# Kernel optimization log

Hardware: AMD Instinct MI355X
Metric: run time of the kernel (lower is better)

The kernel has to match this reference:

```python
import jax, jax.numpy as jnp
import numpy as np

N_HEAD, D_HEAD, D_MODEL = 16, 64, 1024
QLEN, MEMLEN, BSZ = 1024, 1024, 2
KLEN = QLEN + MEMLEN  # rlen == klen
LN_EPS = 1e-5
NEG = -1e30


def _rel_shift(x):
    # x: [qlen, rlen, bsz, n_head] -> Transformer-XL relative shift
    q, r, b, n = x.shape
    zp = jnp.zeros((q, 1, b, n), x.dtype)
    xp = jnp.concatenate([zp, x], axis=1).reshape(r + 1, q, b, n)
    return xp[1:].reshape(q, r, b, n)


def _layer_norm(x, gamma, beta):
    mu = jnp.mean(x, axis=-1, keepdims=True)
    var = jnp.mean((x - mu) ** 2, axis=-1, keepdims=True)
    return (x - mu) * jax.lax.rsqrt(var + LN_EPS) * gamma + beta


def setup_inputs() -> dict:
    key = jax.random.key(0)
    ks = jax.random.split(key, 8)
    w = jax.random.normal(ks[0], (QLEN, BSZ, D_MODEL), jnp.float32)
    r = jax.random.normal(ks[1], (KLEN, D_MODEL), jnp.float32)
    r_w_bias = jax.random.normal(ks[2], (N_HEAD, D_HEAD), jnp.float32) * 0.02
    r_r_bias = jax.random.normal(ks[3], (N_HEAD, D_HEAD), jnp.float32) * 0.02
    mems = jax.random.normal(ks[4], (MEMLEN, BSZ, D_MODEL), jnp.float32)
    W_qkv = jax.random.normal(ks[5], (D_MODEL, 3 * N_HEAD * D_HEAD), jnp.float32) * 0.02
    W_r = jax.random.normal(ks[6], (D_MODEL, N_HEAD * D_HEAD), jnp.float32) * 0.02
    W_o = jax.random.normal(ks[7], (N_HEAD * D_HEAD, D_MODEL), jnp.float32) * 0.02
    ln_gamma = jnp.ones((D_MODEL,), jnp.float32)
    ln_beta = jnp.zeros((D_MODEL,), jnp.float32)
    # causal mask with memory: key j visible to query i iff j <= i + MEMLEN (True = keep)
    attn_mask = jnp.arange(KLEN)[None, :] <= (jnp.arange(QLEN)[:, None] + MEMLEN)
    return {"w": w, "r": r, "r_w_bias": r_w_bias, "r_r_bias": r_r_bias,
            "mems": mems, "attn_mask": attn_mask, "W_qkv": W_qkv, "W_r": W_r,
            "W_o": W_o, "ln_gamma": ln_gamma, "ln_beta": ln_beta}


def reference(w, r, r_w_bias, r_r_bias, mems, attn_mask, W_qkv, W_r, W_o, ln_gamma, ln_beta):
    qlen, bsz = w.shape[0], w.shape[1]
    scale = 1.0 / (D_HEAD ** 0.5)
    cat = jnp.concatenate([mems, w], axis=0)            # [klen, b, d_model]
    klen = cat.shape[0]
    w_heads = cat @ W_qkv                                # [klen, b, 3*H*D]
    r_head_k = (r @ W_r).reshape(-1, N_HEAD, D_HEAD)     # [rlen, H, D]
    w_head_q, w_head_k, w_head_v = jnp.split(w_heads, 3, axis=-1)
    w_head_q = w_head_q[-qlen:].reshape(qlen, bsz, N_HEAD, D_HEAD)
    w_head_k = w_head_k.reshape(klen, bsz, N_HEAD, D_HEAD)
    w_head_v = w_head_v.reshape(klen, bsz, N_HEAD, D_HEAD)
    AC = jnp.einsum('ibnd,jbnd->ijbn', w_head_q + r_w_bias, w_head_k)
    BD = jnp.einsum('ibnd,jnd->ijbn', w_head_q + r_r_bias, r_head_k)
    BD = _rel_shift(BD)
    attn_score = (AC + BD) * scale                       # [q, k, b, n]
    attn_score = jnp.where(attn_mask[:, :, None, None], attn_score, NEG)
    attn_prob = jax.nn.softmax(attn_score, axis=1)
    attn_vec = jnp.einsum('ijbn,jbnd->ibnd', attn_prob, w_head_v)
    attn_vec = attn_vec.reshape(qlen, bsz, N_HEAD * D_HEAD)
    attn_out = attn_vec @ W_o                            # [q, b, d_model]
    return _layer_norm(w + attn_out, ln_gamma, ln_beta)
```

## Files before the change

kernel.cpp:

```cpp
#include <hip/hip_runtime.h>
#include <hip/hip_bf16.h>

#define NHEAD 16
#define DHEAD 64
#define DMODEL 1024
#define QLEN 1024
#define MEMLEN 1024
#define BSZ 2
#define KLEN 2048
#define LN_EPS 1e-5f

typedef __hip_bfloat16 bf16;
typedef __attribute__((ext_vector_type(8))) short short8;
typedef __attribute__((ext_vector_type(4))) float f32x4;

__device__ __forceinline__ float b2f(bf16 x) { return __bfloat162float(x); }
__device__ __forceinline__ bf16 f2b(float x) { return __float2bfloat16(x); }
__device__ __forceinline__ short f2bs(float f) {
    bf16 h = __float2bfloat16(f);
    return *reinterpret_cast<short*>(&h);
}
__device__ __forceinline__ float s2f(short s) {
    bf16 h = *reinterpret_cast<bf16*>(&s);
    return __bfloat162float(h);
}

#define MFMA16(a, b, c) __builtin_amdgcn_mfma_f32_16x16x32_bf16(a, b, c, 0, 0, 0)

#define AS1 __attribute__((address_space(1)))
#define AS3 __attribute__((address_space(3)))
__device__ __forceinline__ void gld16(const bf16* g, bf16* l) {
    __builtin_amdgcn_global_load_lds((const AS1 void*)(uintptr_t)g,
                                     (AS3 void*)(uint32_t)(uintptr_t)l, 16, 0, 0);
}

__global__ __launch_bounds__(256)
void conv_all(const float* __restrict__ mems, const float* __restrict__ w,
              const float* __restrict__ r, bf16* __restrict__ Abf,
              bf16* __restrict__ rbf) {
    const int id = blockIdx.x;
    const float* src;
    bf16* dst;
    int off;
    if (id < 2048)      { src = mems; dst = Abf;                      off = id; }
    else if (id < 4096) { src = w;    dst = Abf + (size_t)2048 * 1024; off = id - 2048; }
    else                { src = r;    dst = rbf;                      off = id - 4096; }
    int i = off * 256 + threadIdx.x;
    const float4 v = reinterpret_cast<const float4*>(src)[i];
    bf16 o[4] = {f2b(v.x), f2b(v.y), f2b(v.z), f2b(v.w)};
    reinterpret_cast<ulong1*>(dst)[i] = *reinterpret_cast<ulong1*>(o);
}

__global__ __launch_bounds__(256)
void conv_wT_all(const float* __restrict__ Wqkv, const float* __restrict__ Wr,
                 const float* __restrict__ Wo, bf16* __restrict__ Wqkvt,
                 bf16* __restrict__ Wrt, bf16* __restrict__ Wot) {
    __shared__ bf16 T[64][65];
    const int id = blockIdx.x;
    const float* in;
    bf16* out;
    int N, tn, tile;
    if (id < 768)       { in = Wqkv; out = Wqkvt; N = 3072; tn = 48; tile = id; }
    else if (id < 1024) { in = Wr;   out = Wrt;   N = 1024; tn = 16; tile = id - 768; }
    else                { in = Wo;   out = Wot;   N = 1024; tn = 16; tile = id - 1024; }
    const int K = 1024;
    const int n0 = (tile % tn) * 64, k0 = (tile / tn) * 64;
    const int t = threadIdx.x;
    #pragma unroll
    for (int e = 0; e < 16; e++) {
        int flat = e * 256 + t;
        int kl = flat >> 6, nl = flat & 63;
        T[kl][nl] = f2b(in[(size_t)(k0 + kl) * N + n0 + nl]);
    }
    __syncthreads();
    #pragma unroll
    for (int e = 0; e < 16; e++) {
        int flat = e * 256 + t;
        int nl = flat >> 6, kl = flat & 63;
        out[(size_t)(n0 + nl) * K + k0 + kl] = T[kl][nl];
    }
}

__global__ __launch_bounds__(256)
void gemm_mfma(const bf16* __restrict__ A, const bf16* __restrict__ Bt,
               const bf16* __restrict__ A2, const bf16* __restrict__ B2,
               int M, int N, int K, int mode,
               const float* __restrict__ rwb, const float* __restrict__ rrb,
               bf16* __restrict__ Qw, bf16* __restrict__ Qr,
               bf16* __restrict__ Kb, bf16* __restrict__ Vb,
               bf16* __restrict__ Cb, float* __restrict__ Cf) {
    const int bm = blockIdx.x * 128, bn = blockIdx.y * 128;
    int sub = 0;
    const bf16* Ap = A;
    const bf16* Bp = Bt;
    if (mode == 0 && bm < 2048 && bn < 1024) { sub = 1; Ap = A2; Bp = B2; }
    __shared__ bf16 As[128 * 32];
    __shared__ bf16 Bs[128 * 32];
    const int t = threadIdx.x;
    const int w = t >> 6, lane = t & 63, quad = lane >> 4, l16 = lane & 15;
    const int wm = (w >> 1) * 64, wn = (w & 1) * 64;
    const int lrow = lane >> 2, lcol = (lane & 3) * 8;

    f32x4 acc[4][4];
    #pragma unroll
    for (int mt = 0; mt < 4; mt++)
        #pragma unroll
        for (int nt = 0; nt < 4; nt++) acc[mt][nt] = (f32x4){0.f, 0.f, 0.f, 0.f};

    for (int k0 = 0; k0 < K; k0 += 32) {
        #pragma unroll
        for (int e = 0; e < 2; e++) {
            int ch = w + 4 * e;
            int row = ch * 16 + lrow;
            gld16(Ap + (size_t)(bm + row) * K + k0 + lcol, As + ch * 512);
            gld16(Bp + (size_t)(bn + row) * K + k0 + lcol, Bs + ch * 512);
        }
        __syncthreads();
        short8 af[4], bfr[4];
        #pragma unroll
        for (int mt = 0; mt < 4; mt++)
            af[mt] = *reinterpret_cast<short8*>(&As[(wm + 16 * mt + l16) * 32 + quad * 8]);
        #pragma unroll
        for (int nt = 0; nt < 4; nt++)
            bfr[nt] = *reinterpret_cast<short8*>(&Bs[(wn + 16 * nt + l16) * 32 + quad * 8]);
        #pragma unroll
        for (int mt = 0; mt < 4; mt++)
            #pragma unroll
            for (int nt = 0; nt < 4; nt++)
                acc[mt][nt] = MFMA16(af[mt], bfr[nt], acc[mt][nt]);
        __syncthreads();
    }

    #pragma unroll
    for (int mt = 0; mt < 4; mt++)
        #pragma unroll
        for (int nt = 0; nt < 4; nt++)
            #pragma unroll
            for (int r = 0; r < 4; r++) {
                int m = bm + wm + 16 * mt + quad * 4 + r;
                int c = bn + wn + 16 * nt + l16;
                float v = acc[mt][nt][r];
                if (sub) {
                    Cb[(size_t)m * 1024 + c] = f2b(v);
                } else if (mode == 0) {
                    int seg = c >> 10, cc = c & 1023;
                    if (seg == 0) {
                        if (m >= 2048) {
                            size_t o = (size_t)(m - 2048) * 1024 + cc;
                            Qw[o] = f2b(v + rwb[cc]);
                            Qr[o] = f2b(v + rrb[cc]);
                        }
                    } else if (seg == 1) Kb[(size_t)m * 1024 + cc] = f2b(v);
                    else                 Vb[(size_t)m * 1024 + cc] = f2b(v);
                } else {
                    Cf[(size_t)m * N + c] = v;
                }
            }
}

__global__ __launch_bounds__(256)
void transpose_v(const bf16* __restrict__ Vb, bf16* __restrict__ Vt) {
    __shared__ bf16 T[64][65];
    const int J0 = blockIdx.x * 64, D0 = blockIdx.y * 64, b = blockIdx.z;
    const int t = threadIdx.x;
    #pragma unroll
    for (int e = 0; e < 16; e++) {
        int flat = e * 256 + t;
        int jl = flat >> 6, dl = flat & 63;
        T[jl][dl] = Vb[(size_t)((J0 + jl) * 2 + b) * 1024 + D0 + dl];
    }
    __syncthreads();
    #pragma unroll
    for (int e = 0; e < 16; e++) {
        int flat = e * 256 + t;
        int dl = flat >> 6, jl = flat & 63;
        Vt[(size_t)((D0 + dl) * 2 + b) * 2048 + J0 + jl] = T[jl][dl];
    }
}

__global__ __launch_bounds__(256, 3)
void attn_mfma(const bf16* __restrict__ Qw, const bf16* __restrict__ Qr,
               const bf16* __restrict__ Kb, const bf16* __restrict__ Vt,
               const bf16* __restrict__ Rk, bf16* __restrict__ Po,
               float* __restrict__ ml) {
    const int id = blockIdx.x;
    const int xcd = id & 7, local = id >> 3;
    const int pair = xcd * 4 + (local & 3);
    const int i0 = (local >> 2) & 15;
    const int js = local >> 6;
    const int b = pair & 1, n = pair >> 1;
    const int I0 = i0 * 64;

    const int tid = threadIdx.x;
    const int w = tid >> 6, lane = tid & 63;
    const int quad = lane >> 4, l16 = lane & 15;
    const int qbase = I0 + 16 * w;
    const int ln8 = lane >> 3;
    const int cs = (lane & 7) ^ (ln8 & 7);
    const int q0 = (quad ^ (l16 & 7)) * 8;
    const int q1 = q0 ^ 32;

    __shared__ bf16 Ks[64 * 64];
    __shared__ bf16 Vs[64 * 64];
    __shared__ bf16 Rs[128 * 64];
    __shared__ short WlB_s[4][16 * 80];
    __shared__ short Pb_s[4][16 * 72];
    short* WlB = WlB_s[w];
    short* Pb = Pb_s[w];

    short8 aqw[2], aqr[2];
    {
        const bf16* qp = Qw + ((size_t)(qbase + l16) * 2 + b) * 1024 + n * 64 + quad * 8;
        aqw[0] = *reinterpret_cast<const short8*>(qp);
        aqw[1] = *reinterpret_cast<const short8*>(qp + 32);
        const bf16* qp2 = Qr + ((size_t)(qbase + l16) * 2 + b) * 1024 + n * 64 + quad * 8;
        aqr[0] = *reinterpret_cast<const short8*>(qp2);
        aqr[1] = *reinterpret_cast<const short8*>(qp2 + 32);
    }

    f32x4 O[4];
    #pragma unroll
    for (int d = 0; d < 4; d++) O[d] = (f32x4){0.f, 0.f, 0.f, 0.f};
    float m_run = -1e30f;
    float pl[4] = {0.f, 0.f, 0.f, 0.f};

    const int T = i0 + 17;
    const int t0 = js ? (T >> 1) : 0;
    const int t1 = js ? T : (T >> 1);
    const int koff = b * 1024 + n * 64 + cs * 8;
    const size_t voff = (size_t)n * 262144 + b * 2048 + cs * 8;
    const int rcol = n * 64 + cs * 8;
    const int rbl = 48 - 16 * w;

    for (int tt = t0; tt < t1; tt++) {
        const int J0 = tt * 64;
        const int RU0 = J0 - I0 + 960;

        #pragma unroll
        for (int e = 0; e < 2; e++) {
            int ch = w + 4 * e;
            int krow = J0 + ch * 8 + ln8;
            gld16(Kb + (size_t)krow * 2048 + koff, Ks + ch * 512);
            int dl = ch * 8 + ln8;
            gld16(Vt + (size_t)dl * 4096 + voff + J0, Vs + ch * 512);
        }
        #pragma unroll
        for (int e = 0; e < 4; e++) {
            int ch = w + 4 * e;
            int rrow = RU0 + ch * 8 + ln8;
            rrow = min(rrow, 2047);
            gld16(Rk + (size_t)rrow * 1024 + rcol, Rs + ch * 512);
        }
        __syncthreads();

        #pragma unroll
        for (int s = 0; s < 5; s++) {
            int rl = rbl + 16 * s + l16;
            short8 b0 = *reinterpret_cast<short8*>(&Rs[rl * 64 + q0]);
            short8 b1 = *reinterpret_cast<short8*>(&Rs[rl * 64 + q1]);
            f32x4 acc = (f32x4){0.f, 0.f, 0.f, 0.f};
            acc = MFMA16(aqr[0], b0, acc);
            acc = MFMA16(aqr[1], b1, acc);
            #pragma unroll
            for (int r = 0; r < 4; r++)
                WlB[(quad * 4 + r) * 80 + 16 * s + l16] = f2bs(acc[r]);
        }

        float sv[4][4];
        #pragma unroll
        for (int n16 = 0; n16 < 4; n16++) {
            int kr = 16 * n16 + l16;
            short8 k0 = *reinterpret_cast<short8*>(&Ks[kr * 64 + q0]);
            short8 k1 = *reinterpret_cast<short8*>(&Ks[kr * 64 + q1]);
            f32x4 acc = (f32x4){0.f, 0.f, 0.f, 0.f};
            acc = MFMA16(aqw[0], k0, acc);
            acc = MFMA16(aqw[1], k1, acc);
            #pragma unroll
            for (int r = 0; r < 4; r++) {
                int row = quad * 4 + r, col = 16 * n16 + l16;
                float s = (acc[r] + s2f(WlB[row * 80 + col - row + 15])) * 0.125f;
                if (J0 + col > qbase + row + MEMLEN) s = -1e30f;
                sv[n16][r] = s;
            }
        }

        float mx = sv[0][0];
        #pragma unroll
        for (int n16 = 0; n16 < 4; n16++)
            #pragma unroll
            for (int r = 0; r < 4; r++) mx = fmaxf(mx, sv[n16][r]);
        #pragma unroll
        for (int msk = 1; msk < 16; msk <<= 1) mx = fmaxf(mx, __shfl_xor(mx, msk));
        const float mn = fmaxf(m_run, mx);
        const float alpha = __expf(m_run - mn);
        m_run = mn;
        #pragma unroll
        for (int n16 = 0; n16 < 4; n16++)
            #pragma unroll
            for (int r = 0; r < 4; r++) sv[n16][r] = __expf(sv[n16][r] - mn);
        #pragma unroll
        for (int r = 0; r < 4; r++)
            pl[r] = pl[r] * alpha + (sv[0][r] + sv[1][r] + sv[2][r] + sv[3][r]);
        #pragma unroll
        for (int d = 0; d < 4; d++)
            #pragma unroll
            for (int r = 0; r < 4; r++) O[d][r] *= alpha;

        #pragma unroll
        for (int n16 = 0; n16 < 4; n16++)
            #pragma unroll
            for (int r = 0; r < 4; r++)
                Pb[(quad * 4 + r) * 72 + 16 * n16 + l16] = f2bs(sv[n16][r]);
        short8 ap0 = *reinterpret_cast<short8*>(&Pb[l16 * 72 + quad * 8]);
        short8 ap1 = *reinterpret_cast<short8*>(&Pb[l16 * 72 + 32 + quad * 8]);

        #pragma unroll
        for (int ds = 0; ds < 4; ds++) {
            int dr = 16 * ds + l16;
            short8 v0 = *reinterpret_cast<short8*>(&Vs[dr * 64 + q0]);
            short8 v1 = *reinterpret_cast<short8*>(&Vs[dr * 64 + q1]);
            O[ds] = MFMA16(ap0, v0, O[ds]);
            O[ds] = MFMA16(ap1, v1, O[ds]);
        }
        __syncthreads();
    }

    float lr[4];
    #pragma unroll
    for (int r = 0; r < 4; r++) {
        float s = pl[r];
        #pragma unroll
        for (int msk = 1; msk < 16; msk <<= 1) s += __shfl_xor(s, msk);
        lr[r] = s;
    }
    #pragma unroll
    for (int ds = 0; ds < 4; ds++)
        #pragma unroll
        for (int r = 0; r < 4; r++) {
            int q = qbase + quad * 4 + r;
            Po[(size_t)js * 2048 * 1024 + ((size_t)q * 2 + b) * 1024
               + n * 64 + 16 * ds + l16] = f2b(O[ds][r] / lr[r]);
        }
    if (l16 == 0) {
        #pragma unroll
        for (int r = 0; r < 4; r++) {
            int q = qbase + quad * 4 + r;
            size_t idx = (((size_t)js * 2048 + q * 2 + b) * 16 + n) * 2;
            ml[idx] = m_run;
            ml[idx + 1] = lr[r];
        }
    }
}

__global__ __launch_bounds__(256)
void combine_attn(const bf16* __restrict__ Po, const float* __restrict__ ml,
                  bf16* __restrict__ AVbf) {
    const int m = blockIdx.x;
    const int t = threadIdx.x;
    #pragma unroll
    for (int e = 0; e < 4; e++) {
        int c = e * 256 + t;
        int n = c >> 6;
        size_t i0 = (((size_t)m) * 16 + n) * 2;
        size_t i1 = (((size_t)2048 + m) * 16 + n) * 2;
        float m0 = ml[i0], l0 = ml[i0 + 1];
        float m1 = ml[i1], l1 = ml[i1 + 1];
        float M = fmaxf(m0, m1);
        float w0 = l0 * __expf(m0 - M), w1 = l1 * __expf(m1 - M);
        float inv = 1.f / (w0 + w1);
        float v = (w0 * b2f(Po[(size_t)m * 1024 + c])
                 + w1 * b2f(Po[(size_t)2048 * 1024 + (size_t)m * 1024 + c])) * inv;
        AVbf[(size_t)m * 1024 + c] = f2b(v);
    }
}

__global__ __launch_bounds__(256)
void ln_res(const float* __restrict__ ao, const float* __restrict__ w,
            const float* __restrict__ gamma, const float* __restrict__ beta,
            float* __restrict__ out) {
    const int m = blockIdx.x;
    const int t = threadIdx.x;
    __shared__ float red[256];
    float x[4];
    #pragma unroll
    for (int e = 0; e < 4; e++) {
        int c = e * 256 + t;
        x[e] = ao[(size_t)m * DMODEL + c] + w[(size_t)m * DMODEL + c];
    }
    float s = x[0] + x[1] + x[2] + x[3];
    red[t] = s;
    __syncthreads();
    #pragma unroll
    for (int off = 128; off; off >>= 1) {
        if (t < off) red[t] += red[t + off];
        __syncthreads();
    }
    const float mu = red[0] * (1.f / 1024.f);
    __syncthreads();
    float s2 = 0.f;
    #pragma unroll
    for (int e = 0; e < 4; e++) { float dx = x[e] - mu; s2 += dx * dx; }
    red[t] = s2;
    __syncthreads();
    #pragma unroll
    for (int off = 128; off; off >>= 1) {
        if (t < off) red[t] += red[t + off];
        __syncthreads();
    }
    const float rstd = rsqrtf(red[0] * (1.f / 1024.f) + LN_EPS);
    #pragma unroll
    for (int e = 0; e < 4; e++) {
        int c = e * 256 + t;
        out[(size_t)m * DMODEL + c] = (x[e] - mu) * rstd * gamma[c] + beta[c];
    }
}

extern "C" void kernel_launch(void* const* d_in, const int* in_sizes, int n_in,
                              void* d_out, int out_size, void* d_ws, size_t ws_size,
                              hipStream_t stream) {
    const float* w        = (const float*)d_in[0];
    const float* r        = (const float*)d_in[1];
    const float* r_w_bias = (const float*)d_in[2];
    const float* r_r_bias = (const float*)d_in[3];
    const float* mems     = (const float*)d_in[4];
    const float* W_qkv    = (const float*)d_in[6];
    const float* W_r      = (const float*)d_in[7];
    const float* W_o      = (const float*)d_in[8];
    const float* gamma    = (const float*)d_in[9];
    const float* beta     = (const float*)d_in[10];
    float* out = (float*)d_out;

    bf16* Abf    = (bf16*)d_ws;
    bf16* Wqkvt  = Abf   + (size_t)4096 * 1024;
    bf16* Wrt    = Wqkvt + (size_t)3072 * 1024;
    bf16* Wot    = Wrt   + (size_t)1024 * 1024;
    bf16* rbf    = Wot   + (size_t)1024 * 1024;
    bf16* Qw     = rbf   + (size_t)2048 * 1024;
    bf16* Qr     = Qw    + (size_t)2048 * 1024;
    bf16* Kb     = Qr    + (size_t)2048 * 1024;
    bf16* Vb     = Kb    + (size_t)4096 * 1024;
    bf16* Vt     = Vb    + (size_t)4096 * 1024;
    bf16* Rk     = Vt    + (size_t)2048 * 2048;
    bf16* AVbf   = Rk    + (size_t)2048 * 1024;
    float* ml    = (float*)(AVbf + (size_t)2048 * 1024);
    bf16* Po     = Abf;
    float* attn_out = (float*)Abf;

    dim3 b256(256);
    conv_all<<<dim3(6144), b256, 0, stream>>>(mems, w, r, Abf, rbf);
    conv_wT_all<<<dim3(1280), b256, 0, stream>>>(W_qkv, W_r, W_o, Wqkvt, Wrt, Wot);
    gemm_mfma<<<dim3(32, 24), b256, 0, stream>>>(
        Abf, Wqkvt, rbf, Wrt, 4096, 3072, 1024, 0, r_w_bias, r_r_bias,
        Qw, Qr, Kb, Vb, Rk, nullptr);
    transpose_v<<<dim3(32, 16, 2), b256, 0, stream>>>(Vb, Vt);
    attn_mfma<<<dim3(1024), b256, 0, stream>>>(Qw, Qr, Kb, Vt, Rk, Po, ml);
    combine_attn<<<dim3(2048), b256, 0, stream>>>(Po, ml, AVbf);
    gemm_mfma<<<dim3(16, 8), b256, 0, stream>>>(
        AVbf, Wot, nullptr, nullptr, 2048, 1024, 1024, 2, nullptr, nullptr,
        nullptr, nullptr, nullptr, nullptr, nullptr, attn_out);
    ln_res<<<dim3(QLEN * BSZ), b256, 0, stream>>>(attn_out, w, gamma, beta, out);
}
```

Measured before the change: 270.1 us.

## Fuse V transpose into GEMM epilogue, drop split-K attention and combine pass

```diff
diff --git a/kernel.cpp b/kernel.cpp
--- a/kernel.cpp
+++ b/kernel.cpp
@@ -35,37 +35,37 @@
 }
 
 __global__ __launch_bounds__(256)
-void conv_all(const float* __restrict__ mems, const float* __restrict__ w,
-              const float* __restrict__ r, bf16* __restrict__ Abf,
-              bf16* __restrict__ rbf) {
-    const int id = blockIdx.x;
-    const float* src;
-    bf16* dst;
-    int off;
-    if (id < 2048)      { src = mems; dst = Abf;                      off = id; }
-    else if (id < 4096) { src = w;    dst = Abf + (size_t)2048 * 1024; off = id - 2048; }
-    else                { src = r;    dst = rbf;                      off = id - 4096; }
-    int i = off * 256 + threadIdx.x;
-    const float4 v = reinterpret_cast<const float4*>(src)[i];
-    bf16 o[4] = {f2b(v.x), f2b(v.y), f2b(v.z), f2b(v.w)};
-    reinterpret_cast<ulong1*>(dst)[i] = *reinterpret_cast<ulong1*>(o);
-}
-
-__global__ __launch_bounds__(256)
-void conv_wT_all(const float* __restrict__ Wqkv, const float* __restrict__ Wr,
-                 const float* __restrict__ Wo, bf16* __restrict__ Wqkvt,
-                 bf16* __restrict__ Wrt, bf16* __restrict__ Wot) {
+void prep(const float* __restrict__ mems, const float* __restrict__ w,
+          const float* __restrict__ r, const float* __restrict__ Wqkv,
+          const float* __restrict__ Wr, const float* __restrict__ Wo,
+          bf16* __restrict__ Abf, bf16* __restrict__ rbf,
+          bf16* __restrict__ Wqkvt, bf16* __restrict__ Wrt,
+          bf16* __restrict__ Wot) {
     __shared__ bf16 T[64][65];
     const int id = blockIdx.x;
+    const int t = threadIdx.x;
+    if (id < 6144) {
+        const float* src;
+        bf16* dst;
+        int off;
+        if (id < 2048)      { src = mems; dst = Abf;                       off = id; }
+        else if (id < 4096) { src = w;    dst = Abf + (size_t)2048 * 1024; off = id - 2048; }
+        else                { src = r;    dst = rbf;                       off = id - 4096; }
+        int i = off * 256 + t;
+        const float4 v = reinterpret_cast<const float4*>(src)[i];
+        bf16 o[4] = {f2b(v.x), f2b(v.y), f2b(v.z), f2b(v.w)};
+        reinterpret_cast<ulong1*>(dst)[i] = *reinterpret_cast<ulong1*>(o);
+        return;
+    }
+    int tid2 = id - 6144;
     const float* in;
     bf16* out;
     int N, tn, tile;
-    if (id < 768)       { in = Wqkv; out = Wqkvt; N = 3072; tn = 48; tile = id; }
-    else if (id < 1024) { in = Wr;   out = Wrt;   N = 1024; tn = 16; tile = id - 768; }
-    else                { in = Wo;   out = Wot;   N = 1024; tn = 16; tile = id - 1024; }
+    if (tid2 < 768)       { in = Wqkv; out = Wqkvt; N = 3072; tn = 48; tile = tid2; }
+    else if (tid2 < 1024) { in = Wr;   out = Wrt;   N = 1024; tn = 16; tile = tid2 - 768; }
+    else                  { in = Wo;   out = Wot;   N = 1024; tn = 16; tile = tid2 - 1024; }
     const int K = 1024;
     const int n0 = (tile % tn) * 64, k0 = (tile / tn) * 64;
-    const int t = threadIdx.x;
     #pragma unroll
     for (int e = 0; e < 16; e++) {
         int flat = e * 256 + t;
@@ -87,7 +87,7 @@
                int M, int N, int K, int mode,
                const float* __restrict__ rwb, const float* __restrict__ rrb,
                bf16* __restrict__ Qw, bf16* __restrict__ Qr,
-               bf16* __restrict__ Kb, bf16* __restrict__ Vb,
+               bf16* __restrict__ Kb, bf16* __restrict__ Vt,
                bf16* __restrict__ Cb, float* __restrict__ Cf) {
     const int bm = blockIdx.x * 128, bn = blockIdx.y * 128;
     int sub = 0;
@@ -150,44 +150,25 @@
                             Qw[o] = f2b(v + rwb[cc]);
                             Qr[o] = f2b(v + rrb[cc]);
                         }
-                    } else if (seg == 1) Kb[(size_t)m * 1024 + cc] = f2b(v);
-                    else                 Vb[(size_t)m * 1024 + cc] = f2b(v);
+                    } else if (seg == 1) {
+                        Kb[(size_t)m * 1024 + cc] = f2b(v);
+                    } else {
+                        Vt[((size_t)cc * 2 + (m & 1)) * 2048 + (m >> 1)] = f2b(v);
+                    }
                 } else {
                     Cf[(size_t)m * N + c] = v;
                 }
             }
 }
 
-__global__ __launch_bounds__(256)
-void transpose_v(const bf16* __restrict__ Vb, bf16* __restrict__ Vt) {
-    __shared__ bf16 T[64][65];
-    const int J0 = blockIdx.x * 64, D0 = blockIdx.y * 64, b = blockIdx.z;
-    const int t = threadIdx.x;
-    #pragma unroll
-    for (int e = 0; e < 16; e++) {
-        int flat = e * 256 + t;
-        int jl = flat >> 6, dl = flat & 63;
-        T[jl][dl] = Vb[(size_t)((J0 + jl) * 2 + b) * 1024 + D0 + dl];
-    }
-    __syncthreads();
-    #pragma unroll
-    for (int e = 0; e < 16; e++) {
-        int flat = e * 256 + t;
-        int dl = flat >> 6, jl = flat & 63;
-        Vt[(size_t)((D0 + dl) * 2 + b) * 2048 + J0 + jl] = T[jl][dl];
-    }
-}
-
 __global__ __launch_bounds__(256, 3)
 void attn_mfma(const bf16* __restrict__ Qw, const bf16* __restrict__ Qr,
                const bf16* __restrict__ Kb, const bf16* __restrict__ Vt,
-               const bf16* __restrict__ Rk, bf16* __restrict__ Po,
-               float* __restrict__ ml) {
+               const bf16* __restrict__ Rk, bf16* __restrict__ AVbf) {
     const int id = blockIdx.x;
     const int xcd = id & 7, local = id >> 3;
     const int pair = xcd * 4 + (local & 3);
-    const int i0 = (local >> 2) & 15;
-    const int js = local >> 6;
+    const int i0 = local >> 2;
     const int b = pair & 1, n = pair >> 1;
     const int I0 = i0 * 64;
 
@@ -225,14 +206,12 @@
     float pl[4] = {0.f, 0.f, 0.f, 0.f};
 
     const int T = i0 + 17;
-    const int t0 = js ? (T >> 1) : 0;
-    const int t1 = js ? T : (T >> 1);
     const int koff = b * 1024 + n * 64 + cs * 8;
     const size_t voff = (size_t)n * 262144 + b * 2048 + cs * 8;
     const int rcol = n * 64 + cs * 8;
     const int rbl = 48 - 16 * w;
 
-    for (int tt = t0; tt < t1; tt++) {
+    for (int tt = 0; tt < T; tt++) {
         const int J0 = tt * 64;
         const int RU0 = J0 - I0 + 960;
 
@@ -338,40 +317,9 @@
         #pragma unroll
         for (int r = 0; r < 4; r++) {
             int q = qbase + quad * 4 + r;
-            Po[(size_t)js * 2048 * 1024 + ((size_t)q * 2 + b) * 1024
-               + n * 64 + 16 * ds + l16] = f2b(O[ds][r] / lr[r]);
-        }
-    if (l16 == 0) {
-        #pragma unroll
-        for (int r = 0; r < 4; r++) {
-            int q = qbase + quad * 4 + r;
-            size_t idx = (((size_t)js * 2048 + q * 2 + b) * 16 + n) * 2;
-            ml[idx] = m_run;
-            ml[idx + 1] = lr[r];
-        }
-    }
-}
-
-__global__ __launch_bounds__(256)
-void combine_attn(const bf16* __restrict__ Po, const float* __restrict__ ml,
-                  bf16* __restrict__ AVbf) {
-    const int m = blockIdx.x;
-    const int t = threadIdx.x;
-    #pragma unroll
-    for (int e = 0; e < 4; e++) {
-        int c = e * 256 + t;
-        int n = c >> 6;
-        size_t i0 = (((size_t)m) * 16 + n) * 2;
-        size_t i1 = (((size_t)2048 + m) * 16 + n) * 2;
-        float m0 = ml[i0], l0 = ml[i0 + 1];
-        float m1 = ml[i1], l1 = ml[i1 + 1];
-        float M = fmaxf(m0, m1);
-        float w0 = l0 * __expf(m0 - M), w1 = l1 * __expf(m1 - M);
-        float inv = 1.f / (w0 + w1);
-        float v = (w0 * b2f(Po[(size_t)m * 1024 + c])
-                 + w1 * b2f(Po[(size_t)2048 * 1024 + (size_t)m * 1024 + c])) * inv;
-        AVbf[(size_t)m * 1024 + c] = f2b(v);
-    }
+            AVbf[((size_t)q * 2 + b) * 1024 + n * 64 + 16 * ds + l16] =
+                f2b(O[ds][r] / lr[r]);
+        }
 }
 
 __global__ __launch_bounds__(256)
@@ -438,23 +386,18 @@
     bf16* Qw     = rbf   + (size_t)2048 * 1024;
     bf16* Qr     = Qw    + (size_t)2048 * 1024;
     bf16* Kb     = Qr    + (size_t)2048 * 1024;
-    bf16* Vb     = Kb    + (size_t)4096 * 1024;
-    bf16* Vt     = Vb    + (size_t)4096 * 1024;
+    bf16* Vt     = Kb    + (size_t)4096 * 1024;
     bf16* Rk     = Vt    + (size_t)2048 * 2048;
     bf16* AVbf   = Rk    + (size_t)2048 * 1024;
-    float* ml    = (float*)(AVbf + (size_t)2048 * 1024);
-    bf16* Po     = Abf;
     float* attn_out = (float*)Abf;
 
     dim3 b256(256);
-    conv_all<<<dim3(6144), b256, 0, stream>>>(mems, w, r, Abf, rbf);
-    conv_wT_all<<<dim3(1280), b256, 0, stream>>>(W_qkv, W_r, W_o, Wqkvt, Wrt, Wot);
+    prep<<<dim3(7424), b256, 0, stream>>>(mems, w, r, W_qkv, W_r, W_o,
+                                          Abf, rbf, Wqkvt, Wrt, Wot);
     gemm_mfma<<<dim3(32, 24), b256, 0, stream>>>(
         Abf, Wqkvt, rbf, Wrt, 4096, 3072, 1024, 0, r_w_bias, r_r_bias,
-        Qw, Qr, Kb, Vb, Rk, nullptr);
-    transpose_v<<<dim3(32, 16, 2), b256, 0, stream>>>(Vb, Vt);
-    attn_mfma<<<dim3(1024), b256, 0, stream>>>(Qw, Qr, Kb, Vt, Rk, Po, ml);
-    combine_attn<<<dim3(2048), b256, 0, stream>>>(Po, ml, AVbf);
+        Qw, Qr, Kb, Vt, Rk, nullptr);
+    attn_mfma<<<dim3(512), b256, 0, stream>>>(Qw, Qr, Kb, Vt, Rk, AVbf);
     gemm_mfma<<<dim3(16, 8), b256, 0, stream>>>(
         AVbf, Wot, nullptr, nullptr, 2048, 1024, 1024, 2, nullptr, nullptr,
         nullptr, nullptr, nullptr, nullptr, nullptr, attn_out);
```

After: 263.4 us. -2.5%, faster.
